# Kernel optimization log

Hardware: AMD Instinct MI355X
Metric: run time of the kernel (lower is better)

Reference implementation:

```python
import jax, jax.numpy as jnp
import numpy as np

EPS = 1e-5


def setup_inputs() -> dict:
    key = jax.random.key(0)
    ks = jax.random.split(key, 8)
    B, C, D, H, O, E = 256, 64, 256, 4096, 256, 4
    x = jax.random.normal(ks[0], (B, C, D), dtype=jnp.float32)
    mask_ids = jax.random.randint(ks[1], (B, C), 0, 16)
    projection_idx = jax.random.randint(ks[2], (C,), 0, E)
    W1 = jax.random.normal(ks[3], (E, D, H), dtype=jnp.float32) * 0.02
    b1 = jnp.zeros((E, H), dtype=jnp.float32)
    gamma = jnp.ones((E, H), dtype=jnp.float32)
    beta = jnp.zeros((E, H), dtype=jnp.float32)
    W2 = jax.random.normal(ks[4], (E, H, O), dtype=jnp.float32) * 0.02
    b2 = jnp.zeros((E, O), dtype=jnp.float32)
    return {"x": x, "mask_ids": mask_ids, "projection_idx": projection_idx,
            "W1": W1, "b1": b1, "gamma": gamma, "beta": beta, "W2": W2, "b2": b2}


def reference(x, mask_ids, projection_idx, W1, b1, gamma, beta, W2, b2):
    # x: [B, C, D]; projection_idx: [C] routes each channel to one of E experts.
    # Disjoint masks => the original zeros + masked '+=' is a partition-assign.
    B, C, D = x.shape
    E, _, H = W1.shape
    # Per-channel expert params (gather once, shared over batch).
    h = jnp.einsum('bcd,cdh->bch', x, W1[projection_idx]) + b1[projection_idx]
    # BatchNorm1d in training mode: batch stats over the tokens of each expert
    # (the original flattens the selected [B, |mask|] tokens for BN).
    seg = jnp.broadcast_to(projection_idx[None, :], (B, C)).reshape(-1)  # [B*C]
    hf = h.reshape(B * C, H)
    cnt = jax.ops.segment_sum(jnp.ones((B * C,), h.dtype), seg, num_segments=E)
    cnt = jnp.maximum(cnt, 1.0)
    s1 = jax.ops.segment_sum(hf, seg, num_segments=E)            # [E, H]
    s2 = jax.ops.segment_sum(hf * hf, seg, num_segments=E)       # [E, H]
    mean = s1 / cnt[:, None]
    var = s2 / cnt[:, None] - mean * mean                        # biased var (train-mode BN)
    inv = jax.lax.rsqrt(var + EPS)
    hn = (h - mean[projection_idx]) * (inv[projection_idx] * gamma[projection_idx]) + beta[projection_idx]
    a = jax.nn.relu(hn)
    out = jnp.einsum('bch,cho->bco', a, W2[projection_idx]) + b2[projection_idx]
    return out, mask_ids
```

## Files before the change

### kernel.cpp

```cpp
#include <hip/hip_runtime.h>

typedef unsigned short u16;
typedef unsigned int   u32;
typedef __attribute__((ext_vector_type(8))) short s16x8;
typedef __attribute__((ext_vector_type(4))) float f32x4;
typedef __attribute__((ext_vector_type(4))) u32   u32x4;

#define DEV static __device__ __forceinline__

static constexpr int B_ = 256, C_ = 64, D_ = 256, H_ = 4096, O_ = 256, E_ = 4;

DEV u16 f2bf(float f) {
  u32 u = __builtin_bit_cast(u32, f);
  u += 0x7fffu + ((u >> 16) & 1u);
  return (u16)(u >> 16);
}
DEV float bf2f(u16 u) { return __builtin_bit_cast(float, (u32)u << 16); }

DEV void async16(const u16* g, u16* l) {
  __builtin_amdgcn_global_load_lds(
      (const __attribute__((address_space(1))) void*)g,
      (__attribute__((address_space(3))) void*)l, 16, 0, 0);
}

DEV int xcd_swz(int bid, int nwg) { return (bid & 7) * (nwg >> 3) + (bid >> 3); }

__global__ void k_prep(const float* __restrict__ x, u16* __restrict__ xb,
                       const float* __restrict__ W1, u16* __restrict__ w1t,
                       const float* __restrict__ W2, u16* __restrict__ w2t,
                       const int* __restrict__ proj, int* __restrict__ perm) {
  __shared__ float tile[64][65];
  const int bx = blockIdx.x, tid = threadIdx.x;
  if (bx < 2048) {
    const int i = bx * 256 + tid;
    const f32x4 a = ((const f32x4*)x)[2 * i];
    const f32x4 b = ((const f32x4*)x)[2 * i + 1];
    u32x4 o;
    o[0] = (u32)f2bf(a[0]) | ((u32)f2bf(a[1]) << 16);
    o[1] = (u32)f2bf(a[2]) | ((u32)f2bf(a[3]) << 16);
    o[2] = (u32)f2bf(b[0]) | ((u32)f2bf(b[1]) << 16);
    o[3] = (u32)f2bf(b[2]) | ((u32)f2bf(b[3]) << 16);
    ((u32x4*)xb)[i] = o;
    return;
  }
  if (bx < 4096) {
    const bool w1 = bx < 3072;
    const int R  = w1 ? D_ : H_;
    const int Cc = w1 ? H_ : O_;
    const float* s0 = w1 ? W1 : W2;
    u16* d0 = w1 ? w1t : w2t;
    int b = bx - (w1 ? 2048 : 3072);
    const int nct = Cc >> 6, nrt = R >> 6;
    const int ct = b % nct; b /= nct;
    const int rt = b % nrt; const int e = b / nrt;
    const float* s = s0 + (size_t)e * R * Cc;
    u16* d = d0 + (size_t)e * R * Cc;
    const int tx = tid & 63, ty = tid >> 6;
    #pragma unroll
    for (int i = 0; i < 64; i += 4)
      tile[i + ty][tx] = s[(size_t)(rt * 64 + i + ty) * Cc + ct * 64 + tx];
    __syncthreads();
    #pragma unroll
    for (int i = 0; i < 64; i += 4) {
      const int cc = i + ty;
      d[(size_t)(ct * 64 + cc) * R + rt * 64 + tx] = f2bf(tile[tx][cc]);
    }
    return;
  }
  if (tid < C_) {
    const int e = proj[tid];
    int rank = 0;
    for (int c2 = 0; c2 < C_; ++c2) {
      const int e2 = proj[c2];
      rank += (e2 < e) || (e2 == e && c2 < tid);
    }
    perm[rank] = tid;
  }
}

__global__ __launch_bounds__(256, 4)
void k_gemm1(const u16* __restrict__ A, const u16* __restrict__ Bw,
             const int* __restrict__ proj, const int* __restrict__ perm,
             const float* __restrict__ bias,
             u16* __restrict__ outH, float* __restrict__ s1p, float* __restrict__ s2p) {
  constexpr int BM = 128, BN = 128, BK = 32, KT = D_ / BK;
  constexpr int SA = BM * BK / 8, SB = BN * BK / 8;
  constexpr int BUF = (SA + SB) * 8;
  __shared__ __align__(16) u16 lds[2 * BUF];
  __shared__ float stash[2][4][16][2];
  const int tid = threadIdx.x, l = tid & 63, w = tid >> 6, wm = w >> 1, wn = w & 1;

  int bid = xcd_swz(blockIdx.x, gridDim.x);
  constexpr int NT = H_ / BN, BT = B_ / BM;
  const int nt = bid % NT; bid /= NT;
  const int bt = bid % BT; const int ci = bid / BT;
  const int c = perm[ci];
  const int e = proj[c];

  const size_t rsA = (size_t)C_ * D_;
  const u16* Ab = A + (size_t)c * D_ + (size_t)bt * BM * rsA;
  const u16* Bb = Bw + ((size_t)e * H_ + (size_t)nt * BN) * D_;

  f32x4 acc[4][4] = {};

  auto stage = [&](int kt) {
    const int k0 = kt * BK;
    u16* dst = lds + (kt & 1) * BUF;
    #pragma unroll
    for (int i = 0; i < 2; ++i) {
      const int s = i * 256 + tid, row = s >> 2, j = (s & 3) ^ ((row >> 1) & 3);
      async16(Ab + (size_t)row * rsA + k0 + j * 8, dst + s * 8);
    }
    #pragma unroll
    for (int i = 0; i < 2; ++i) {
      const int s = i * 256 + tid, col = s >> 2, j = (s & 3) ^ ((col >> 1) & 3);
      async16(Bb + (size_t)col * D_ + k0 + j * 8, dst + SA * 8 + s * 8);
    }
  };

  stage(0);
  asm volatile("s_waitcnt vmcnt(0)" ::: "memory");
  __builtin_amdgcn_s_barrier();

  #pragma unroll
  for (int kt = 0; kt < KT; ++kt) {
    if (kt + 1 < KT) stage(kt + 1);
    const u16* bufA = lds + (kt & 1) * BUF;
    const u16* bufB = bufA + SA * 8;
    s16x8 av[4], bv[4];
    #pragma unroll
    for (int m = 0; m < 4; ++m) {
      const int r = wm * 64 + m * 16 + (l & 15), p = (l >> 4) ^ ((r >> 1) & 3);
      av[m] = *(const s16x8*)(bufA + (r * 4 + p) * 8);
    }
    #pragma unroll
    for (int n = 0; n < 4; ++n) {
      const int cc = wn * 64 + n * 16 + (l & 15), p = (l >> 4) ^ ((cc >> 1) & 3);
      bv[n] = *(const s16x8*)(bufB + (cc * 4 + p) * 8);
    }
    #pragma unroll
    for (int m = 0; m < 4; ++m)
      #pragma unroll
      for (int n = 0; n < 4; ++n)
        acc[m][n] = __builtin_amdgcn_mfma_f32_16x16x32_bf16(av[m], bv[n], acc[m][n], 0, 0, 0);
    asm volatile("s_waitcnt vmcnt(0) lgkmcnt(0)" ::: "memory");
    __builtin_amdgcn_s_barrier();
  }

  u16* ldsOut = lds;
  float p1s[4], p2s[4];
  #pragma unroll
  for (int n = 0; n < 4; ++n) {
    const int colL = wn * 64 + n * 16 + (l & 15);
    const int colg = nt * BN + colL;
    const float bval = bias[e * H_ + colg];
    float p1 = 0.f, p2 = 0.f;
    #pragma unroll
    for (int m = 0; m < 4; ++m) {
      const int rbase = wm * 64 + m * 16 + (l >> 4) * 4;
      #pragma unroll
      for (int i = 0; i < 4; ++i) {
        const float v = acc[m][n][i] + bval;
        p1 += v; p2 += v * v;
        const int row = rbase + i;
        const int phys = (colL >> 3) ^ (row & 15);
        ldsOut[row * 128 + phys * 8 + (colL & 7)] = f2bf(v);
      }
    }
    p1 += __shfl_xor(p1, 16); p1 += __shfl_xor(p1, 32);
    p2 += __shfl_xor(p2, 16); p2 += __shfl_xor(p2, 32);
    if (wm == 1 && l < 16) { stash[wn][n][l & 15][0] = p1; stash[wn][n][l & 15][1] = p2; }
    p1s[n] = p1; p2s[n] = p2;
  }
  __syncthreads();
  if (wm == 0 && l < 16) {
    const int rowp = c * 2 + bt;
    #pragma unroll
    for (int n = 0; n < 4; ++n) {
      const int colg = nt * BN + wn * 64 + n * 16 + (l & 15);
      s1p[(size_t)rowp * H_ + colg] = p1s[n] + stash[wn][n][l & 15][0];
      s2p[(size_t)rowp * H_ + colg] = p2s[n] + stash[wn][n][l & 15][1];
    }
  }
  u16* outB = outH + ((size_t)c * B_ + (size_t)bt * BM) * H_ + nt * BN;
  #pragma unroll
  for (int pass = 0; pass < 8; ++pass) {
    const int row = pass * 16 + (tid >> 4), sl = tid & 15;
    const u32x4 v = *(const u32x4*)(ldsOut + row * 128 + ((sl ^ (row & 15)) * 8));
    *(u32x4*)(outB + (size_t)row * H_ + sl * 8) = v;
  }
}

__global__ void k_finalize(const float* __restrict__ s1p, const float* __restrict__ s2p,
                           const int* __restrict__ proj, const float* __restrict__ gamma,
                           const float* __restrict__ beta,
                           u16* __restrict__ sclB, u16* __restrict__ shfB) {
  const int i = blockIdx.x * 256 + threadIdx.x;
  const int e = i >> 12;
  const int hcol = i & 4095;
  int cn = 0;
  float q1 = 0.f, q2 = 0.f;
  for (int c = 0; c < C_; ++c) {
    if (proj[c] == e) {
      ++cn;
      q1 += s1p[(size_t)(c * 2) * H_ + hcol] + s1p[(size_t)(c * 2 + 1) * H_ + hcol];
      q2 += s2p[(size_t)(c * 2) * H_ + hcol] + s2p[(size_t)(c * 2 + 1) * H_ + hcol];
    }
  }
  const float cnt = fmaxf((float)cn * (float)B_, 1.f);
  const float mean = q1 / cnt;
  const float var = q2 / cnt - mean * mean;
  const float sc = rsqrtf(var + 1e-5f) * gamma[i];
  sclB[i] = f2bf(sc);
  shfB[i] = f2bf(beta[i] - mean * sc);
}

template<int KS>
__global__ __launch_bounds__(256, 2)
void k_gemm2(const u16* __restrict__ A, const u16* __restrict__ Bw,
             const int* __restrict__ proj, const int* __restrict__ perm,
             const float* __restrict__ b2,
             const u16* __restrict__ scB, const u16* __restrict__ shB,
             float* __restrict__ outF, float* __restrict__ partial) {
  constexpr int BM = 64, BN = 256, BK = 32, KH = H_ / KS, KT = KH / BK;
  constexpr int SA = BM * BK / 8, SB = BN * BK / 8;
  constexpr int BUF = (SA + SB) * 8;
  __shared__ __align__(16) u16 lds[2 * BUF + 2 * KH];
  u16* stS = lds + 2 * BUF;
  u16* stT = stS + KH;
  const int tid = threadIdx.x, l = tid & 63, w = tid >> 6;

  int bid = xcd_swz(blockIdx.x, gridDim.x);
  const int ks = bid & (KS - 1); bid /= KS;
  const int bt = bid & 3; const int ci = bid >> 2;
  const int c = perm[ci];
  const int e = proj[c];

  const u16* Ab = A + ((size_t)c * B_ + (size_t)bt * BM) * H_ + (size_t)ks * KH;
  const u16* Bb = Bw + (size_t)e * O_ * H_ + (size_t)ks * KH;
  const u16* scE = scB + e * H_ + ks * KH;
  const u16* shE = shB + e * H_ + ks * KH;

  f32x4 acc[4][4] = {};
  s16x8 h0[1], h1[1], b0r[4], b1r[4];

  auto Aissue = [&](int kt, s16x8 (&hs)[1]) {
    const int k0 = kt * BK;
    const int s = tid, row = s >> 2, j = (s & 3) ^ ((row >> 1) & 3);
    hs[0] = *(const s16x8*)(Ab + (size_t)row * H_ + k0 + j * 8);
  };
  auto Bissue = [&](int kt, s16x8 (&bs)[4]) {
    const int k0 = kt * BK;
    #pragma unroll
    for (int i = 0; i < 4; ++i) {
      const int s = i * 256 + tid, col = s >> 2, j = (s & 3) ^ ((col >> 1) & 3);
      bs[i] = *(const s16x8*)(Bb + (size_t)col * H_ + k0 + j * 8);
    }
  };
  auto Awrite = [&](int kt, s16x8 (&hs)[1]) {
    u16* dst = lds + (kt & 1) * BUF;
    const int k0 = kt * BK;
    const int s = tid, j = (s & 3) ^ (((s >> 2) >> 1) & 3);
    const s16x8 sv = *(const s16x8*)(stS + k0 + j * 8);
    const s16x8 tv = *(const s16x8*)(stT + k0 + j * 8);
    u32x4 o;
    #pragma unroll
    for (int jj = 0; jj < 4; ++jj) {
      const float v0 = fmaxf(bf2f((u16)hs[0][2 * jj]) * bf2f((u16)sv[2 * jj]) + bf2f((u16)tv[2 * jj]), 0.f);
      const float v1 = fmaxf(bf2f((u16)hs[0][2 * jj + 1]) * bf2f((u16)sv[2 * jj + 1]) + bf2f((u16)tv[2 * jj + 1]), 0.f);
      o[jj] = (u32)f2bf(v0) | ((u32)f2bf(v1) << 16);
    }
    *(u32x4*)(dst + s * 8) = o;
  };
  auto Bwrite = [&](int kt, s16x8 (&bs)[4]) {
    u16* dst = lds + (kt & 1) * BUF + SA * 8;
    #pragma unroll
    for (int i = 0; i < 4; ++i) {
      const int s = i * 256 + tid;
      *(u32x4*)(dst + s * 8) = __builtin_bit_cast(u32x4, bs[i]);
    }
  };
  auto Compute = [&](int kt) {
    const u16* bufA = lds + (kt & 1) * BUF;
    const u16* bufB = bufA + SA * 8;
    s16x8 av[4], bv[4];
    #pragma unroll
    for (int m = 0; m < 4; ++m) {
      const int r = m * 16 + (l & 15), p = (l >> 4) ^ ((r >> 1) & 3);
      av[m] = *(const s16x8*)(bufA + (r * 4 + p) * 8);
    }
    #pragma unroll
    for (int n = 0; n < 4; ++n) {
      const int cc = w * 64 + n * 16 + (l & 15), p = (l >> 4) ^ ((cc >> 1) & 3);
      bv[n] = *(const s16x8*)(bufB + (cc * 4 + p) * 8);
    }
    #pragma unroll
    for (int m = 0; m < 4; ++m)
      #pragma unroll
      for (int n = 0; n < 4; ++n)
        acc[m][n] = __builtin_amdgcn_mfma_f32_16x16x32_bf16(av[m], bv[n], acc[m][n], 0, 0, 0);
  };

  for (int q = tid; q < KH / 4; q += 256) {
    if (q < KH / 8) async16(scE + q * 8, stS + q * 8);
    else            async16(shE + (q - KH / 8) * 8, stT + (q - KH / 8) * 8);
  }
  Aissue(0, h0); Bissue(0, b0r);
  Aissue(1, h1); Bissue(1, b1r);
  asm volatile("s_waitcnt vmcnt(0)" ::: "memory");
  __builtin_amdgcn_s_barrier();
  Awrite(0, h0); Bwrite(0, b0r);
  asm volatile("s_waitcnt lgkmcnt(0)" ::: "memory");
  __builtin_amdgcn_s_barrier();

  #pragma unroll 1
  for (int kt = 0; kt + 3 < KT; kt += 2) {
    Aissue(kt + 2, h0); Bissue(kt + 2, b0r);
    Compute(kt);
    Awrite(kt + 1, h1); Bwrite(kt + 1, b1r);
    asm volatile("s_waitcnt lgkmcnt(0)" ::: "memory");
    __builtin_amdgcn_s_barrier();
    Aissue(kt + 3, h1); Bissue(kt + 3, b1r);
    Compute(kt + 1);
    Awrite(kt + 2, h0); Bwrite(kt + 2, b0r);
    asm volatile("s_waitcnt lgkmcnt(0)" ::: "memory");
    __builtin_amdgcn_s_barrier();
  }

  Compute(KT - 2);
  Awrite(KT - 1, h1); Bwrite(KT - 1, b1r);
  asm volatile("s_waitcnt lgkmcnt(0)" ::: "memory");
  __builtin_amdgcn_s_barrier();
  Compute(KT - 1);

  float* dstF = ks ? partial : outF;
  #pragma unroll
  for (int n = 0; n < 4; ++n) {
    const int colg = w * 64 + n * 16 + (l & 15);
    const float bval = ks ? 0.f : b2[e * O_ + colg];
    #pragma unroll
    for (int m = 0; m < 4; ++m) {
      #pragma unroll
      for (int i = 0; i < 4; ++i) {
        const int rg = bt * BM + m * 16 + (l >> 4) * 4 + i;
        dstF[((size_t)rg * C_ + c) * O_ + colg] = acc[m][n][i] + bval;
      }
    }
  }
}

__global__ void k_combine(float* __restrict__ out, const float* __restrict__ partial,
                          const int* __restrict__ mask, float* __restrict__ maskOut) {
  const int gi = blockIdx.x * 256 + threadIdx.x;
  const size_t b = (size_t)gi * 2;
  f32x4 a0 = ((const f32x4*)out)[b], a1 = ((const f32x4*)out)[b + 1];
  const f32x4 p0 = ((const f32x4*)partial)[b], p1 = ((const f32x4*)partial)[b + 1];
  #pragma unroll
  for (int j = 0; j < 4; ++j) { a0[j] += p0[j]; a1[j] += p1[j]; }
  ((f32x4*)out)[b] = a0; ((f32x4*)out)[b + 1] = a1;
  if (gi < B_ * C_ / 8) {
    #pragma unroll
    for (int j = 0; j < 8; ++j) maskOut[gi * 8 + j] = (float)mask[gi * 8 + j];
  }
}

extern "C" void kernel_launch(void* const* d_in, const int* in_sizes, int n_in,
                              void* d_out, int out_size, void* d_ws, size_t ws_size,
                              hipStream_t stream) {
  const float* x     = (const float*)d_in[0];
  const int*   mask  = (const int*)d_in[1];
  const int*   proj  = (const int*)d_in[2];
  const float* W1    = (const float*)d_in[3];
  const float* b1    = (const float*)d_in[4];
  const float* gamma = (const float*)d_in[5];
  const float* beta  = (const float*)d_in[6];
  const float* W2    = (const float*)d_in[7];
  const float* b2    = (const float*)d_in[8];
  float* out = (float*)d_out;

  char* ws = (char*)d_ws;
  size_t off = 0;
  u16* hbuf = (u16*)(ws + off); off += (size_t)B_ * C_ * H_ * 2;
  u16* xb   = (u16*)(ws + off); off += (size_t)B_ * C_ * D_ * 2;
  u16* w1t  = (u16*)(ws + off); off += (size_t)E_ * D_ * H_ * 2;
  float* partial = (float*)xb;
  u16* w2t  = (u16*)(ws + off); off += (size_t)E_ * H_ * O_ * 2;
  float* s1p = (float*)(ws + off); off += (size_t)2 * C_ * H_ * 4;
  float* s2p = (float*)(ws + off); off += (size_t)2 * C_ * H_ * 4;
  u16* sclB = (u16*)(ws + off); off += (size_t)E_ * H_ * 2;
  u16* shfB = (u16*)(ws + off); off += (size_t)E_ * H_ * 2;
  int* perm = (int*)(ws + off); off += 256;


  k_prep<<<4097, 256, 0, stream>>>(x, xb, W1, w1t, W2, w2t, proj, perm);

  k_gemm1<<<C_ * 2 * 32, 256, 0, stream>>>(xb, w1t, proj, perm, b1, hbuf, s1p, s2p);

  k_finalize<<<E_ * H_ / 256, 256, 0, stream>>>(s1p, s2p, proj, gamma, beta, sclB, shfB);

  k_gemm2<2><<<512, 256, 0, stream>>>(hbuf, w2t, proj, perm, b2, sclB, shfB, out, partial);

  k_combine<<<B_ * C_ * O_ / 8 / 256, 256, 0, stream>>>(out, partial, mask,
                                                        out + (size_t)B_ * C_ * O_);
}
```

Measured before the change: 158.4 us.

## Drop split-K in second GEMM, tile hidden buffer by column block, fold mask copy

```diff
diff --git a/kernel.cpp b/kernel.cpp
--- a/kernel.cpp
+++ b/kernel.cpp
@@ -28,6 +28,7 @@
 __global__ void k_prep(const float* __restrict__ x, u16* __restrict__ xb,
                        const float* __restrict__ W1, u16* __restrict__ w1t,
                        const float* __restrict__ W2, u16* __restrict__ w2t,
+                       const int* __restrict__ mask, float* __restrict__ maskOut,
                        const int* __restrict__ proj, int* __restrict__ perm) {
   __shared__ float tile[64][65];
   const int bx = blockIdx.x, tid = threadIdx.x;
@@ -67,6 +68,12 @@
     }
     return;
   }
+  if (bx < 4104) {
+    const int i = (bx - 4096) * 256 + tid;
+    #pragma unroll
+    for (int j = 0; j < 8; ++j) maskOut[i * 8 + j] = (float)mask[i * 8 + j];
+    return;
+  }
   if (tid < C_) {
     const int e = proj[tid];
     int rank = 0;
@@ -182,12 +189,12 @@
       s2p[(size_t)rowp * H_ + colg] = p2s[n] + stash[wn][n][l & 15][1];
     }
   }
-  u16* outB = outH + ((size_t)c * B_ + (size_t)bt * BM) * H_ + nt * BN;
+  u16* outB = outH + (((size_t)c * NT + nt) * B_ + (size_t)bt * BM) * 128;
   #pragma unroll
   for (int pass = 0; pass < 8; ++pass) {
     const int row = pass * 16 + (tid >> 4), sl = tid & 15;
     const u32x4 v = *(const u32x4*)(ldsOut + row * 128 + ((sl ^ (row & 15)) * 8));
-    *(u32x4*)(outB + (size_t)row * H_ + sl * 8) = v;
+    *(u32x4*)(outB + (size_t)row * 128 + sl * 8) = v;
   }
 }
 
@@ -215,39 +222,40 @@
   shfB[i] = f2bf(beta[i] - mean * sc);
 }
 
-template<int KS>
-__global__ __launch_bounds__(256, 2)
+__global__ __launch_bounds__(256, 3)
 void k_gemm2(const u16* __restrict__ A, const u16* __restrict__ Bw,
              const int* __restrict__ proj, const int* __restrict__ perm,
              const float* __restrict__ b2,
              const u16* __restrict__ scB, const u16* __restrict__ shB,
-             float* __restrict__ outF, float* __restrict__ partial) {
-  constexpr int BM = 64, BN = 256, BK = 32, KH = H_ / KS, KT = KH / BK;
+             float* __restrict__ outF) {
+  constexpr int BM = 32, BN = 256, BK = 32, KT = H_ / BK;
   constexpr int SA = BM * BK / 8, SB = BN * BK / 8;
   constexpr int BUF = (SA + SB) * 8;
-  __shared__ __align__(16) u16 lds[2 * BUF + 2 * KH];
+  __shared__ __align__(16) u16 lds[2 * BUF + 2 * H_];
   u16* stS = lds + 2 * BUF;
-  u16* stT = stS + KH;
+  u16* stT = stS + H_;
   const int tid = threadIdx.x, l = tid & 63, w = tid >> 6;
 
   int bid = xcd_swz(blockIdx.x, gridDim.x);
-  const int ks = bid & (KS - 1); bid /= KS;
-  const int bt = bid & 3; const int ci = bid >> 2;
+  const int bt = bid & 7; const int ci = bid >> 3;
   const int c = perm[ci];
   const int e = proj[c];
 
-  const u16* Ab = A + ((size_t)c * B_ + (size_t)bt * BM) * H_ + (size_t)ks * KH;
-  const u16* Bb = Bw + (size_t)e * O_ * H_ + (size_t)ks * KH;
-  const u16* scE = scB + e * H_ + ks * KH;
-  const u16* shE = shB + e * H_ + ks * KH;
-
-  f32x4 acc[4][4] = {};
-  s16x8 h0[1], h1[1], b0r[4], b1r[4];
-
-  auto Aissue = [&](int kt, s16x8 (&hs)[1]) {
-    const int k0 = kt * BK;
-    const int s = tid, row = s >> 2, j = (s & 3) ^ ((row >> 1) & 3);
-    hs[0] = *(const s16x8*)(Ab + (size_t)row * H_ + k0 + j * 8);
+  const u16* Ab = A + (size_t)c * 32 * B_ * 128 + (size_t)bt * BM * 128;
+  const u16* Bb = Bw + (size_t)e * O_ * H_;
+  const u16* scE = scB + e * H_;
+  const u16* shE = shB + e * H_;
+
+  f32x4 acc[2][4] = {};
+  s16x8 h0, h1, b0r[4], b1r[4];
+
+  auto Aissue = [&](int kt, s16x8& hs) {
+    if (tid < 128) {
+      const int k0 = kt * BK;
+      const int row = tid >> 2, j = (tid & 3) ^ ((row >> 1) & 3);
+      const int k = k0 + j * 8;
+      hs = *(const s16x8*)(Ab + (size_t)(k >> 7) * (B_ * 128) + row * 128 + (k & 127));
+    }
   };
   auto Bissue = [&](int kt, s16x8 (&bs)[4]) {
     const int k0 = kt * BK;
@@ -257,20 +265,22 @@
       bs[i] = *(const s16x8*)(Bb + (size_t)col * H_ + k0 + j * 8);
     }
   };
-  auto Awrite = [&](int kt, s16x8 (&hs)[1]) {
-    u16* dst = lds + (kt & 1) * BUF;
-    const int k0 = kt * BK;
-    const int s = tid, j = (s & 3) ^ (((s >> 2) >> 1) & 3);
-    const s16x8 sv = *(const s16x8*)(stS + k0 + j * 8);
-    const s16x8 tv = *(const s16x8*)(stT + k0 + j * 8);
-    u32x4 o;
-    #pragma unroll
-    for (int jj = 0; jj < 4; ++jj) {
-      const float v0 = fmaxf(bf2f((u16)hs[0][2 * jj]) * bf2f((u16)sv[2 * jj]) + bf2f((u16)tv[2 * jj]), 0.f);
-      const float v1 = fmaxf(bf2f((u16)hs[0][2 * jj + 1]) * bf2f((u16)sv[2 * jj + 1]) + bf2f((u16)tv[2 * jj + 1]), 0.f);
-      o[jj] = (u32)f2bf(v0) | ((u32)f2bf(v1) << 16);
-    }
-    *(u32x4*)(dst + s * 8) = o;
+  auto Awrite = [&](int kt, s16x8& hs) {
+    if (tid < 128) {
+      u16* dst = lds + (kt & 1) * BUF;
+      const int k0 = kt * BK;
+      const int row = tid >> 2, j = (tid & 3) ^ ((row >> 1) & 3);
+      const s16x8 sv = *(const s16x8*)(stS + k0 + j * 8);
+      const s16x8 tv = *(const s16x8*)(stT + k0 + j * 8);
+      u32x4 o;
+      #pragma unroll
+      for (int jj = 0; jj < 4; ++jj) {
+        const float v0 = fmaxf(bf2f((u16)hs[2 * jj]) * bf2f((u16)sv[2 * jj]) + bf2f((u16)tv[2 * jj]), 0.f);
+        const float v1 = fmaxf(bf2f((u16)hs[2 * jj + 1]) * bf2f((u16)sv[2 * jj + 1]) + bf2f((u16)tv[2 * jj + 1]), 0.f);
+        o[jj] = (u32)f2bf(v0) | ((u32)f2bf(v1) << 16);
+      }
+      *(u32x4*)(dst + tid * 8) = o;
+    }
   };
   auto Bwrite = [&](int kt, s16x8 (&bs)[4]) {
     u16* dst = lds + (kt & 1) * BUF + SA * 8;
@@ -283,9 +293,9 @@
   auto Compute = [&](int kt) {
     const u16* bufA = lds + (kt & 1) * BUF;
     const u16* bufB = bufA + SA * 8;
-    s16x8 av[4], bv[4];
-    #pragma unroll
-    for (int m = 0; m < 4; ++m) {
+    s16x8 av[2], bv[4];
+    #pragma unroll
+    for (int m = 0; m < 2; ++m) {
       const int r = m * 16 + (l & 15), p = (l >> 4) ^ ((r >> 1) & 3);
       av[m] = *(const s16x8*)(bufA + (r * 4 + p) * 8);
     }
@@ -295,15 +305,15 @@
       bv[n] = *(const s16x8*)(bufB + (cc * 4 + p) * 8);
     }
     #pragma unroll
-    for (int m = 0; m < 4; ++m)
+    for (int m = 0; m < 2; ++m)
       #pragma unroll
       for (int n = 0; n < 4; ++n)
         acc[m][n] = __builtin_amdgcn_mfma_f32_16x16x32_bf16(av[m], bv[n], acc[m][n], 0, 0, 0);
   };
 
-  for (int q = tid; q < KH / 4; q += 256) {
-    if (q < KH / 8) async16(scE + q * 8, stS + q * 8);
-    else            async16(shE + (q - KH / 8) * 8, stT + (q - KH / 8) * 8);
+  for (int q = tid; q < H_ / 4; q += 256) {
+    if (q < H_ / 8) async16(scE + q * 8, stS + q * 8);
+    else            async16(shE + (q - H_ / 8) * 8, stT + (q - H_ / 8) * 8);
   }
   Aissue(0, h0); Bissue(0, b0r);
   Aissue(1, h1); Bissue(1, b1r);
@@ -333,34 +343,18 @@
   __builtin_amdgcn_s_barrier();
   Compute(KT - 1);
 
-  float* dstF = ks ? partial : outF;
   #pragma unroll
   for (int n = 0; n < 4; ++n) {
     const int colg = w * 64 + n * 16 + (l & 15);
-    const float bval = ks ? 0.f : b2[e * O_ + colg];
-    #pragma unroll
-    for (int m = 0; m < 4; ++m) {
+    const float bval = b2[e * O_ + colg];
+    #pragma unroll
+    for (int m = 0; m < 2; ++m) {
       #pragma unroll
       for (int i = 0; i < 4; ++i) {
         const int rg = bt * BM + m * 16 + (l >> 4) * 4 + i;
-        dstF[((size_t)rg * C_ + c) * O_ + colg] = acc[m][n][i] + bval;
+        outF[((size_t)rg * C_ + c) * O_ + colg] = acc[m][n][i] + bval;
       }
     }
-  }
-}
-
-__global__ void k_combine(float* __restrict__ out, const float* __restrict__ partial,
-                          const int* __restrict__ mask, float* __restrict__ maskOut) {
-  const int gi = blockIdx.x * 256 + threadIdx.x;
-  const size_t b = (size_t)gi * 2;
-  f32x4 a0 = ((const f32x4*)out)[b], a1 = ((const f32x4*)out)[b + 1];
-  const f32x4 p0 = ((const f32x4*)partial)[b], p1 = ((const f32x4*)partial)[b + 1];
-  #pragma unroll
-  for (int j = 0; j < 4; ++j) { a0[j] += p0[j]; a1[j] += p1[j]; }
-  ((f32x4*)out)[b] = a0; ((f32x4*)out)[b + 1] = a1;
-  if (gi < B_ * C_ / 8) {
-    #pragma unroll
-    for (int j = 0; j < 8; ++j) maskOut[gi * 8 + j] = (float)mask[gi * 8 + j];
   }
 }
 
@@ -383,7 +377,6 @@
   u16* hbuf = (u16*)(ws + off); off += (size_t)B_ * C_ * H_ * 2;
   u16* xb   = (u16*)(ws + off); off += (size_t)B_ * C_ * D_ * 2;
   u16* w1t  = (u16*)(ws + off); off += (size_t)E_ * D_ * H_ * 2;
-  float* partial = (float*)xb;
   u16* w2t  = (u16*)(ws + off); off += (size_t)E_ * H_ * O_ * 2;
   float* s1p = (float*)(ws + off); off += (size_t)2 * C_ * H_ * 4;
   float* s2p = (float*)(ws + off); off += (size_t)2 * C_ * H_ * 4;
@@ -392,14 +385,12 @@
   int* perm = (int*)(ws + off); off += 256;
 
 
-  k_prep<<<4097, 256, 0, stream>>>(x, xb, W1, w1t, W2, w2t, proj, perm);
+  k_prep<<<4105, 256, 0, stream>>>(x, xb, W1, w1t, W2, w2t, mask,
+                                   out + (size_t)B_ * C_ * O_, proj, perm);
 
   k_gemm1<<<C_ * 2 * 32, 256, 0, stream>>>(xb, w1t, proj, perm, b1, hbuf, s1p, s2p);
 
   k_finalize<<<E_ * H_ / 256, 256, 0, stream>>>(s1p, s2p, proj, gamma, beta, sclB, shfB);
 
-  k_gemm2<2><<<512, 256, 0, stream>>>(hbuf, w2t, proj, perm, b2, sclB, shfB, out, partial);
-
-  k_combine<<<B_ * C_ * O_ / 8 / 256, 256, 0, stream>>>(out, partial, mask,
-                                                        out + (size_t)B_ * C_ * O_);
-}
+  k_gemm2<<<512, 256, 0, stream>>>(hbuf, w2t, proj, perm, b2, sclB, shfB, out);
+}
```

Result: slower. 177.1 us (+11.8%).

## Triple-buffer gemm1 K loop, tile hidden buffer layout, move mask cast to prep

Applied to the files above, without the earlier changes.

```diff
diff --git a/kernel.cpp b/kernel.cpp
--- a/kernel.cpp
+++ b/kernel.cpp
@@ -28,6 +28,7 @@
 __global__ void k_prep(const float* __restrict__ x, u16* __restrict__ xb,
                        const float* __restrict__ W1, u16* __restrict__ w1t,
                        const float* __restrict__ W2, u16* __restrict__ w2t,
+                       const int* __restrict__ mask, float* __restrict__ maskOut,
                        const int* __restrict__ proj, int* __restrict__ perm) {
   __shared__ float tile[64][65];
   const int bx = blockIdx.x, tid = threadIdx.x;
@@ -67,6 +68,12 @@
     }
     return;
   }
+  if (bx < 4104) {
+    const int i = (bx - 4096) * 256 + tid;
+    #pragma unroll
+    for (int j = 0; j < 8; ++j) maskOut[i * 8 + j] = (float)mask[i * 8 + j];
+    return;
+  }
   if (tid < C_) {
     const int e = proj[tid];
     int rank = 0;
@@ -78,7 +85,7 @@
   }
 }
 
-__global__ __launch_bounds__(256, 4)
+__global__ __launch_bounds__(256, 3)
 void k_gemm1(const u16* __restrict__ A, const u16* __restrict__ Bw,
              const int* __restrict__ proj, const int* __restrict__ perm,
              const float* __restrict__ bias,
@@ -86,7 +93,7 @@
   constexpr int BM = 128, BN = 128, BK = 32, KT = D_ / BK;
   constexpr int SA = BM * BK / 8, SB = BN * BK / 8;
   constexpr int BUF = (SA + SB) * 8;
-  __shared__ __align__(16) u16 lds[2 * BUF];
+  __shared__ __align__(16) u16 lds[3 * BUF];
   __shared__ float stash[2][4][16][2];
   const int tid = threadIdx.x, l = tid & 63, w = tid >> 6, wm = w >> 1, wn = w & 1;
 
@@ -105,7 +112,7 @@
 
   auto stage = [&](int kt) {
     const int k0 = kt * BK;
-    u16* dst = lds + (kt & 1) * BUF;
+    u16* dst = lds + (kt % 3) * BUF;
     #pragma unroll
     for (int i = 0; i < 2; ++i) {
       const int s = i * 256 + tid, row = s >> 2, j = (s & 3) ^ ((row >> 1) & 3);
@@ -119,13 +126,15 @@
   };
 
   stage(0);
-  asm volatile("s_waitcnt vmcnt(0)" ::: "memory");
+  asm volatile("" ::: "memory");
+  stage(1);
+  asm volatile("s_waitcnt vmcnt(4)" ::: "memory");
   __builtin_amdgcn_s_barrier();
 
   #pragma unroll
   for (int kt = 0; kt < KT; ++kt) {
-    if (kt + 1 < KT) stage(kt + 1);
-    const u16* bufA = lds + (kt & 1) * BUF;
+    if (kt + 2 < KT) stage(kt + 2);
+    const u16* bufA = lds + (kt % 3) * BUF;
     const u16* bufB = bufA + SA * 8;
     s16x8 av[4], bv[4];
     #pragma unroll
@@ -143,9 +152,11 @@
       #pragma unroll
       for (int n = 0; n < 4; ++n)
         acc[m][n] = __builtin_amdgcn_mfma_f32_16x16x32_bf16(av[m], bv[n], acc[m][n], 0, 0, 0);
-    asm volatile("s_waitcnt vmcnt(0) lgkmcnt(0)" ::: "memory");
-    __builtin_amdgcn_s_barrier();
-  }
+    if (kt + 2 < KT)      asm volatile("s_waitcnt vmcnt(4) lgkmcnt(0)" ::: "memory");
+    else if (kt + 1 < KT) asm volatile("s_waitcnt vmcnt(0) lgkmcnt(0)" ::: "memory");
+    if (kt + 1 < KT) __builtin_amdgcn_s_barrier();
+  }
+  __syncthreads();
 
   u16* ldsOut = lds;
   float p1s[4], p2s[4];
@@ -182,12 +193,12 @@
       s2p[(size_t)rowp * H_ + colg] = p2s[n] + stash[wn][n][l & 15][1];
     }
   }
-  u16* outB = outH + ((size_t)c * B_ + (size_t)bt * BM) * H_ + nt * BN;
+  u16* outB = outH + (((size_t)c * NT + nt) * B_ + (size_t)bt * BM) * 128;
   #pragma unroll
   for (int pass = 0; pass < 8; ++pass) {
     const int row = pass * 16 + (tid >> 4), sl = tid & 15;
     const u32x4 v = *(const u32x4*)(ldsOut + row * 128 + ((sl ^ (row & 15)) * 8));
-    *(u32x4*)(outB + (size_t)row * H_ + sl * 8) = v;
+    *(u32x4*)(outB + (size_t)row * 128 + sl * 8) = v;
   }
 }
 
@@ -215,13 +226,13 @@
   shfB[i] = f2bf(beta[i] - mean * sc);
 }
 
-template<int KS>
 __global__ __launch_bounds__(256, 2)
 void k_gemm2(const u16* __restrict__ A, const u16* __restrict__ Bw,
              const int* __restrict__ proj, const int* __restrict__ perm,
              const float* __restrict__ b2,
              const u16* __restrict__ scB, const u16* __restrict__ shB,
              float* __restrict__ outF, float* __restrict__ partial) {
+  constexpr int KS = 2;
   constexpr int BM = 64, BN = 256, BK = 32, KH = H_ / KS, KT = KH / BK;
   constexpr int SA = BM * BK / 8, SB = BN * BK / 8;
   constexpr int BUF = (SA + SB) * 8;
@@ -231,12 +242,12 @@
   const int tid = threadIdx.x, l = tid & 63, w = tid >> 6;
 
   int bid = xcd_swz(blockIdx.x, gridDim.x);
-  const int ks = bid & (KS - 1); bid /= KS;
+  const int ks = bid & 1; bid >>= 1;
   const int bt = bid & 3; const int ci = bid >> 2;
   const int c = perm[ci];
   const int e = proj[c];
 
-  const u16* Ab = A + ((size_t)c * B_ + (size_t)bt * BM) * H_ + (size_t)ks * KH;
+  const u16* Ab = A + ((size_t)c * 32 * B_ + (size_t)bt * BM) * 128;
   const u16* Bb = Bw + (size_t)e * O_ * H_ + (size_t)ks * KH;
   const u16* scE = scB + e * H_ + ks * KH;
   const u16* shE = shB + e * H_ + ks * KH;
@@ -245,9 +256,9 @@
   s16x8 h0[1], h1[1], b0r[4], b1r[4];
 
   auto Aissue = [&](int kt, s16x8 (&hs)[1]) {
-    const int k0 = kt * BK;
-    const int s = tid, row = s >> 2, j = (s & 3) ^ ((row >> 1) & 3);
-    hs[0] = *(const s16x8*)(Ab + (size_t)row * H_ + k0 + j * 8);
+    const int row = tid >> 2, j = (tid & 3) ^ ((row >> 1) & 3);
+    const int kg = ks * KH + kt * BK + j * 8;
+    hs[0] = *(const s16x8*)(Ab + (size_t)(kg >> 7) * (B_ * 128) + row * 128 + (kg & 127));
   };
   auto Bissue = [&](int kt, s16x8 (&bs)[4]) {
     const int k0 = kt * BK;
@@ -260,7 +271,7 @@
   auto Awrite = [&](int kt, s16x8 (&hs)[1]) {
     u16* dst = lds + (kt & 1) * BUF;
     const int k0 = kt * BK;
-    const int s = tid, j = (s & 3) ^ (((s >> 2) >> 1) & 3);
+    const int row = tid >> 2, j = (tid & 3) ^ ((row >> 1) & 3);
     const s16x8 sv = *(const s16x8*)(stS + k0 + j * 8);
     const s16x8 tv = *(const s16x8*)(stT + k0 + j * 8);
     u32x4 o;
@@ -270,7 +281,7 @@
       const float v1 = fmaxf(bf2f((u16)hs[0][2 * jj + 1]) * bf2f((u16)sv[2 * jj + 1]) + bf2f((u16)tv[2 * jj + 1]), 0.f);
       o[jj] = (u32)f2bf(v0) | ((u32)f2bf(v1) << 16);
     }
-    *(u32x4*)(dst + s * 8) = o;
+    *(u32x4*)(dst + tid * 8) = o;
   };
   auto Bwrite = [&](int kt, s16x8 (&bs)[4]) {
     u16* dst = lds + (kt & 1) * BUF + SA * 8;
@@ -349,8 +360,7 @@
   }
 }
 
-__global__ void k_combine(float* __restrict__ out, const float* __restrict__ partial,
-                          const int* __restrict__ mask, float* __restrict__ maskOut) {
+__global__ void k_combine(float* __restrict__ out, const float* __restrict__ partial) {
   const int gi = blockIdx.x * 256 + threadIdx.x;
   const size_t b = (size_t)gi * 2;
   f32x4 a0 = ((const f32x4*)out)[b], a1 = ((const f32x4*)out)[b + 1];
@@ -358,10 +368,6 @@
   #pragma unroll
   for (int j = 0; j < 4; ++j) { a0[j] += p0[j]; a1[j] += p1[j]; }
   ((f32x4*)out)[b] = a0; ((f32x4*)out)[b + 1] = a1;
-  if (gi < B_ * C_ / 8) {
-    #pragma unroll
-    for (int j = 0; j < 8; ++j) maskOut[gi * 8 + j] = (float)mask[gi * 8 + j];
-  }
 }
 
 extern "C" void kernel_launch(void* const* d_in, const int* in_sizes, int n_in,
@@ -391,15 +397,14 @@
   u16* shfB = (u16*)(ws + off); off += (size_t)E_ * H_ * 2;
   int* perm = (int*)(ws + off); off += 256;
 
-
-  k_prep<<<4097, 256, 0, stream>>>(x, xb, W1, w1t, W2, w2t, proj, perm);
+  k_prep<<<4105, 256, 0, stream>>>(x, xb, W1, w1t, W2, w2t, mask,
+                                   out + (size_t)B_ * C_ * O_, proj, perm);
 
   k_gemm1<<<C_ * 2 * 32, 256, 0, stream>>>(xb, w1t, proj, perm, b1, hbuf, s1p, s2p);
 
   k_finalize<<<E_ * H_ / 256, 256, 0, stream>>>(s1p, s2p, proj, gamma, beta, sclB, shfB);
 
-  k_gemm2<2><<<512, 256, 0, stream>>>(hbuf, w2t, proj, perm, b2, sclB, shfB, out, partial);
-
-  k_combine<<<B_ * C_ * O_ / 8 / 256, 256, 0, stream>>>(out, partial, mask,
-                                                        out + (size_t)B_ * C_ * O_);
-}
+  k_gemm2<<<512, 256, 0, stream>>>(hbuf, w2t, proj, perm, b2, sclB, shfB, out, partial);
+
+  k_combine<<<B_ * C_ * O_ / 8 / 256, 256, 0, stream>>>(out, partial);
+}
```

After: 151.9 us, median of 3. -4.1%, faster.
